# Kernel tuning notes

Measured on AMD Instinct MI355X. Metric: run time of the kernel, lower is better.

Reference implementation:

```python
import jax, jax.numpy as jnp
import numpy as np

SOFTMAX_SCALE = 10.0  # self.softmax_scale
EPS = 1e-4


def _patches(img, k=3):
    # img: [H, W, C] -> patches laid out as conv filters [k, k, C, L], L = H*W
    # (matches tf.image.extract_patches SAME/stride1 + reshape + transpose([0,2,3,4,1]))
    H, W, C = img.shape
    pad = (k - 1) // 2
    xp = jnp.pad(img, ((pad, pad), (pad, pad), (0, 0)))
    pat = jnp.stack([jnp.stack([xp[p:p + H, q:q + W] for q in range(k)]) for p in range(k)])
    # pat: [k, k, H, W, C] -> [k, k, C, H*W]; L index is row-major (h*W + w) like TF reshape
    return pat.transpose(0, 1, 4, 2, 3).reshape(k, k, C, H * W)


def _normed(p):
    # per-patch L2 normalization over the k*k*C axes (axes 0,1,2)
    return p / jnp.maximum(jnp.sqrt(jnp.sum(p * p, axis=(0, 1, 2))), EPS)


def _corr_recon(a, b, k=3):
    # a, b: [H', W', C] shifted feature maps
    Hp, Wp, C = a.shape
    L = Hp * Wp
    pa = _patches(a, k)  # [k,k,C,L]
    pb = _patches(b, k)
    y = (_normed(pa) * _normed(pb)).reshape(k * k * C, L)
    att = y.T @ y                                   # [L, L] patch-correlation scores
    att = jax.nn.softmax(att.reshape(1, Hp, Wp, L) * SOFTMAX_SCALE, axis=3)
    dn = ('NHWC', 'HWIO', 'NHWC')
    # tf.nn.conv2d_transpose(att, filters=[k,k,C,L], stride=1, SAME); rate=1 so /rate**2 is a no-op
    ya = jax.lax.conv_transpose(att, pa, (1, 1), 'SAME', dimension_numbers=dn, transpose_kernel=True)[0]
    yb = jax.lax.conv_transpose(att, pb, (1, 1), 'SAME', dimension_numbers=dn, transpose_kernel=True)[0]
    return ya, yb  # each [H', W', C]


def _ecattn_single(xi):
    # xi: [H, W, C]
    left, right = xi[:-1], xi[1:]          # vertical neighbor pair, [H-1, W, C]
    top, bottom = xi[:, 1:], xi[:, :-1]    # horizontal neighbor pair, [H, W-1, C]
    yl, yr = _corr_recon(left, right)
    ylr = jnp.concatenate([yr[:1], (yr[1:] + yl[:-1]) * 0.5, yl[-1:]], axis=0)   # [H, W, C]
    yt, yb = _corr_recon(top, bottom)
    ytb = jnp.concatenate([yt[:, :1], (yt[:, 1:] + yb[:, :-1]) * 0.5, yb[:, -1:]], axis=1)  # [H, W, C]
    return (ylr + ytb) * 0.5


def setup_inputs() -> dict:
    key = jax.random.key(0)
    k1, k2 = jax.random.split(key)
    B, H, W, C = 4, 32, 32, 256
    x = jax.random.normal(k1, (B, H, W, C), dtype=jnp.float32)
    mask = jax.random.uniform(k2, (B, H, W, 1), dtype=jnp.float32)
    return {'x': x, 'mask': mask}


def reference(x, mask):
    # mask is accepted by the layer's call() but unused inside contextualAttention
    return jax.vmap(_ecattn_single)(x)
```

## Files before the change

kernel.cpp:

```cpp
#include <hip/hip_runtime.h>


typedef _Float16 half8 __attribute__((ext_vector_type(8)));
typedef _Float16 half8u __attribute__((ext_vector_type(8), aligned(4)));
typedef _Float16 half4h __attribute__((ext_vector_type(4)));
typedef _Float16 half4u __attribute__((ext_vector_type(4), aligned(8)));
typedef float floatx4 __attribute__((ext_vector_type(4)));

constexpr int NL = 992, NC = 256, NC2 = 512;
constexpr int NLL = NL * NL;
constexpr int OFF_ABT = 0;
constexpr int OFF_MH  = OFF_ABT + NL * NC2 / 2;
constexpr int OFF_SA  = OFF_MH + NL * NC / 2;
constexpr int OFF_SB  = OFF_SA + 1024;
constexpr int OFF_INV = OFF_SA + 2048;
constexpr int OFF_Y   = OFF_SA + 3072;
constexpr int OFF_B0  = OFF_Y + NL * NC2 / 2;
constexpr int OFF_B1  = OFF_B0 + NLL / 2;
constexpr int TSTRIDE = OFF_B1 + NLL / 2;

__device__ __forceinline__ void gload16(const void* g, void* l) {
    __builtin_amdgcn_global_load_lds(
        (const __attribute__((address_space(1))) unsigned int*)g,
        (__attribute__((address_space(3))) unsigned int*)(unsigned long)(uintptr_t)l,
        16, 0, 0);
}

__global__ __launch_bounds__(256) void k_stage(const float* __restrict__ x,
                                               float* __restrict__ ws) {
    const int t = blockIdx.x & 7;
    const int l0 = (blockIdx.x >> 3) * 32;
    const int s = t >> 1, o = t & 1;
    float* wst = ws + (size_t)t * TSTRIDE;
    _Float16* __restrict__ ABt = (_Float16*)(wst + OFF_ABT);
    _Float16* __restrict__ Mh = (_Float16*)(wst + OFF_MH);
    __shared__ float Ta[32 * 33], Tb[32 * 33];
    const int tid = threadIdx.x;
    const int li = tid >> 3, cq = tid & 7;
    const int l = l0 + li;
    int aoff, boff;
    if (o == 0) {
        const int lh = l >> 5, lw = l & 31;
        aoff = ((s * 32 + lh) * 32 + lw) * NC;
        boff = aoff + 32 * NC;
    } else {
        const int lh = l / 31, lw = l - lh * 31;
        boff = ((s * 32 + lh) * 32 + lw) * NC;
        aoff = boff + NC;
    }
    float sa = 0.0f, sb = 0.0f;
    for (int cc = 0; cc < 8; ++cc) {
        const int c0 = cc * 32;
        const float4 a4 = *(const float4*)&x[aoff + c0 + cq * 4];
        const float4 b4 = *(const float4*)&x[boff + c0 + cq * 4];
        half4h m;
        m[0] = (_Float16)(a4.x * b4.x); m[1] = (_Float16)(a4.y * b4.y);
        m[2] = (_Float16)(a4.z * b4.z); m[3] = (_Float16)(a4.w * b4.w);
        *(half4u*)&Mh[l * NC + c0 + cq * 4] = m;
        sa += a4.x * a4.x + a4.y * a4.y + a4.z * a4.z + a4.w * a4.w;
        sb += b4.x * b4.x + b4.y * b4.y + b4.z * b4.z + b4.w * b4.w;
        __syncthreads();
        Ta[(cq * 4 + 0) * 33 + li] = a4.x; Tb[(cq * 4 + 0) * 33 + li] = b4.x;
        Ta[(cq * 4 + 1) * 33 + li] = a4.y; Tb[(cq * 4 + 1) * 33 + li] = b4.y;
        Ta[(cq * 4 + 2) * 33 + li] = a4.z; Tb[(cq * 4 + 2) * 33 + li] = b4.z;
        Ta[(cq * 4 + 3) * 33 + li] = a4.w; Tb[(cq * 4 + 3) * 33 + li] = b4.w;
        __syncthreads();
        const int ci = li, lq = cq;
        half4h ha, hb;
#pragma unroll
        for (int j = 0; j < 4; ++j) {
            ha[j] = (_Float16)Ta[ci * 33 + lq * 4 + j];
            hb[j] = (_Float16)Tb[ci * 33 + lq * 4 + j];
        }
        *(half4u*)&ABt[(c0 + ci) * NL + l0 + lq * 4] = ha;
        *(half4u*)&ABt[(NC + c0 + ci) * NL + l0 + lq * 4] = hb;
    }
#pragma unroll
    for (int off = 4; off > 0; off >>= 1) {
        sa += __shfl_down(sa, off, 8);
        sb += __shfl_down(sb, off, 8);
    }
    if (cq == 0) {
        wst[OFF_SA + l] = sa;
        wst[OFF_SB + l] = sb;
    }
}

__global__ __launch_bounds__(256) void k_gram(float* __restrict__ ws) {
    const int t = blockIdx.x & 7;
    const int u = blockIdx.x >> 3;
    const int i0 = (u >> 4) * 64, j0 = (u & 15) * 64;
    float* wst = ws + (size_t)t * TSTRIDE;
    const _Float16* __restrict__ M = (const _Float16*)(wst + OFF_MH);
    _Float16* __restrict__ S = (_Float16*)(wst + OFF_B0);
    const int tid = threadIdx.x;

    if (u == 0) {
        const int o = t & 1;
        const int Hp = o ? 32 : 31, Wp = o ? 31 : 32;
#pragma unroll
        for (int q = 0; q < 4; ++q) {
            const int l = tid + q * 256;
            if (l < NL) {
                const int h = l / Wp, w = l - h * Wp;
                float na2 = 0.0f, nb2 = 0.0f;
#pragma unroll
                for (int dh = -1; dh <= 1; ++dh)
#pragma unroll
                    for (int dw = -1; dw <= 1; ++dw) {
                        const int hh = h + dh, ww = w + dw;
                        if ((unsigned)hh < (unsigned)Hp && (unsigned)ww < (unsigned)Wp) {
                            const int ll = hh * Wp + ww;
                            na2 += wst[OFF_SA + ll];
                            nb2 += wst[OFF_SB + ll];
                        }
                    }
                const float na = fmaxf(sqrtf(na2), 1e-4f);
                const float nb = fmaxf(sqrtf(nb2), 1e-4f);
                wst[OFF_INV + l] = 1.0f / (na * nb);
            }
        }
    }

    __shared__ __align__(16) _Float16 As[64 * 64];
    __shared__ __align__(16) _Float16 Bs[64 * 64];
    const int wave = tid >> 6, lane = tid & 63;
    const int wm = wave & 1, wn = wave >> 1;
    const int l15 = lane & 15, quad = lane >> 4;
    floatx4 acc[2][2] = {};
    for (int k0 = 0; k0 < NC; k0 += 64) {
        __syncthreads();
#pragma unroll
        for (int rr = 0; rr < 2; ++rr) {
            const int slot = tid + rr * 256;
            const int row = slot >> 3, cg = (slot & 7) * 8;
            if (i0 + row < NL) gload16(&M[(i0 + row) * NC + k0 + cg], &As[row * 64 + cg]);
            if (j0 + row < NL) gload16(&M[(j0 + row) * NC + k0 + cg], &Bs[row * 64 + cg]);
        }
        __syncthreads();
#pragma unroll
        for (int kk = 0; kk < 2; ++kk) {
            half8 a[2], b[2];
#pragma unroll
            for (int mt = 0; mt < 2; ++mt) a[mt] = *(const half8*)&As[(wm * 32 + mt * 16 + l15) * 64 + kk * 32 + quad * 8];
#pragma unroll
            for (int nt = 0; nt < 2; ++nt) b[nt] = *(const half8*)&Bs[(wn * 32 + nt * 16 + l15) * 64 + kk * 32 + quad * 8];
#pragma unroll
            for (int mt = 0; mt < 2; ++mt)
#pragma unroll
                for (int nt = 0; nt < 2; ++nt)
                    acc[mt][nt] = __builtin_amdgcn_mfma_f32_16x16x32_f16(a[mt], b[nt], acc[mt][nt], 0, 0, 0);
        }
    }
#pragma unroll
    for (int mt = 0; mt < 2; ++mt)
#pragma unroll
        for (int nt = 0; nt < 2; ++nt)
#pragma unroll
            for (int r = 0; r < 4; ++r) {
                const int row = i0 + wm * 32 + mt * 16 + quad * 4 + r;
                const int col = j0 + wn * 32 + nt * 16 + l15;
                if (row < NL && col < NL) S[row * NL + col] = (_Float16)acc[mt][nt][r];
            }
}

template<int WP, int HP>
__device__ __forceinline__ void softmax9_body(float* __restrict__ wst,
                                              const int l1, const int tid) {
    const _Float16* __restrict__ S = (const _Float16*)(wst + OFF_B0);
    const float* __restrict__ inv = wst + OFF_INV;
    _Float16* __restrict__ Ph = (_Float16*)(wst + OFF_B1);
    const int c0 = tid * 4;
    const int h1 = l1 / WP, w1 = l1 % WP;
    float lg[4] = {-3.0e38f, -3.0e38f, -3.0e38f, -3.0e38f};
    float mx = -3.0e38f;
    if (tid < 248) {
        int hc[4], wc[4];
#pragma unroll
        for (int j = 0; j < 4; ++j) { hc[j] = (c0 + j) / WP; wc[j] = (c0 + j) % WP; }
        float g[4] = {0.f, 0.f, 0.f, 0.f};
        const _Float16* base = S + l1 * NL + c0;
#pragma unroll
        for (int dh = -1; dh <= 1; ++dh) {
            const bool oh1 = (unsigned)(h1 + dh) < (unsigned)HP;
#pragma unroll
            for (int dw = -1; dw <= 1; ++dw) {
                const int sh = dh * WP + dw;
                const int par = sh & 1;
                const bool ok1 = oh1 && (unsigned)(w1 + dw) < (unsigned)WP;
                const half8u v = *(const half8u*)(base + sh * (NL + 1) - par);
#pragma unroll
                for (int j = 0; j < 4; ++j) {
                    const bool ok = ok1 && (unsigned)(hc[j] + dh) < (unsigned)HP &&
                                           (unsigned)(wc[j] + dw) < (unsigned)WP;
                    if (ok) g[j] += (float)v[j + par];
                }
            }
        }
        const float inv1 = inv[l1] * 10.0f;
#pragma unroll
        for (int j = 0; j < 4; ++j) {
            lg[j] = g[j] * inv1 * inv[c0 + j];
            mx = fmaxf(mx, lg[j]);
        }
    }
    __shared__ float red[4];
    const int wave = tid >> 6, lane = tid & 63;
#pragma unroll
    for (int off = 32; off > 0; off >>= 1) mx = fmaxf(mx, __shfl_down(mx, off));
    if (lane == 0) red[wave] = mx;
    __syncthreads();
    mx = fmaxf(fmaxf(red[0], red[1]), fmaxf(red[2], red[3]));
    __syncthreads();
    float e[4];
    float sum = 0.0f;
#pragma unroll
    for (int j = 0; j < 4; ++j) { e[j] = __expf(lg[j] - mx); sum += e[j]; }
    if (tid >= 248) sum = 0.0f;
#pragma unroll
    for (int off = 32; off > 0; off >>= 1) sum += __shfl_down(sum, off);
    if (lane == 0) red[wave] = sum;
    __syncthreads();
    sum = red[0] + red[1] + red[2] + red[3];
    const float rs = 1.0f / sum;
    if (tid < 248) {
        half4h o;
#pragma unroll
        for (int j = 0; j < 4; ++j) o[j] = (_Float16)(e[j] * rs);
        *(half4u*)(Ph + l1 * NL + c0) = o;
    }
}

__global__ __launch_bounds__(256) void k_softmax9(float* __restrict__ ws) {
    const int t = blockIdx.x & 7;
    const int l1 = blockIdx.x >> 3;
    float* wst = ws + (size_t)t * TSTRIDE;
    if (t & 1) softmax9_body<31, 32>(wst, l1, threadIdx.x);
    else       softmax9_body<32, 31>(wst, l1, threadIdx.x);
}

template<int WP, int HP>
__device__ __forceinline__ void band9p_body(float* __restrict__ wst,
                                            const int m, const int tid) {
    if (tid >= 248) return;
    const _Float16* __restrict__ P = (const _Float16*)(wst + OFF_B1);
    _Float16* __restrict__ W = (_Float16*)(wst + OFF_B0);
    const int c0 = tid * 4;
    const int hm = m / WP, wm = m % WP;
    int hc[4], wc[4];
#pragma unroll
    for (int j = 0; j < 4; ++j) { hc[j] = (c0 + j) / WP; wc[j] = (c0 + j) % WP; }
    float acc[4] = {0.f, 0.f, 0.f, 0.f};
    const _Float16* base = P + m * NL + c0;
#pragma unroll
    for (int dh = -1; dh <= 1; ++dh) {
        const bool oh1 = (unsigned)(hm + dh) < (unsigned)HP;
#pragma unroll
        for (int dw = -1; dw <= 1; ++dw) {
            const int sh = dh * WP + dw;
            const int par = sh & 1;
            const bool ok1 = oh1 && (unsigned)(wm + dw) < (unsigned)WP;
            const half8u v = *(const half8u*)(base + sh * (NL + 1) - par);
#pragma unroll
            for (int j = 0; j < 4; ++j) {
                const bool ok = ok1 && (unsigned)(hc[j] + dh) < (unsigned)HP &&
                                       (unsigned)(wc[j] + dw) < (unsigned)WP;
                if (ok) acc[j] += (float)v[j + par];
            }
        }
    }
    half4h o;
#pragma unroll
    for (int j = 0; j < 4; ++j) o[j] = (_Float16)acc[j];
    *(half4u*)(W + m * NL + c0) = o;
}

__global__ __launch_bounds__(256) void k_band9p(float* __restrict__ ws) {
    const int t = blockIdx.x & 7;
    const int m = blockIdx.x >> 3;
    float* wst = ws + (size_t)t * TSTRIDE;
    if (t & 1) band9p_body<31, 32>(wst, m, threadIdx.x);
    else       band9p_body<32, 31>(wst, m, threadIdx.x);
}

__global__ __launch_bounds__(256) void k_recon(float* __restrict__ ws) {
    const int t = blockIdx.x & 7;
    const int u = blockIdx.x >> 3;
    const int i0 = (u >> 3) * 64, j0 = (u & 7) * 64;
    float* wst = ws + (size_t)t * TSTRIDE;
    const _Float16* __restrict__ Wm = (const _Float16*)(wst + OFF_B0);
    const _Float16* __restrict__ ABt = (const _Float16*)(wst + OFF_ABT);
    _Float16* __restrict__ Y = (_Float16*)(wst + OFF_Y);
    __shared__ __align__(16) _Float16 As[64 * 32];
    __shared__ __align__(16) _Float16 Bs[64 * 32];
    const int tid = threadIdx.x;
    const int wave = tid >> 6, lane = tid & 63;
    const int wm = wave & 1, wn = wave >> 1;
    const int l15 = lane & 15, quad = lane >> 4;
    floatx4 acc[2][2] = {};
    const int row = tid >> 2, cg = (tid & 3) * 8;
    for (int k0 = 0; k0 < NL; k0 += 32) {
        __syncthreads();
        if (i0 + row < NL) gload16(&Wm[(i0 + row) * NL + k0 + cg], &As[row * 32 + cg]);
        gload16(&ABt[(j0 + row) * NL + k0 + cg], &Bs[row * 32 + cg]);
        __syncthreads();
        half8 a[2], b[2];
#pragma unroll
        for (int mt = 0; mt < 2; ++mt) a[mt] = *(const half8*)&As[(wm * 32 + mt * 16 + l15) * 32 + quad * 8];
#pragma unroll
        for (int nt = 0; nt < 2; ++nt) b[nt] = *(const half8*)&Bs[(wn * 32 + nt * 16 + l15) * 32 + quad * 8];
#pragma unroll
        for (int mt = 0; mt < 2; ++mt)
#pragma unroll
            for (int nt = 0; nt < 2; ++nt)
                acc[mt][nt] = __builtin_amdgcn_mfma_f32_16x16x32_f16(a[mt], b[nt], acc[mt][nt], 0, 0, 0);
    }
#pragma unroll
    for (int mt = 0; mt < 2; ++mt)
#pragma unroll
        for (int nt = 0; nt < 2; ++nt)
#pragma unroll
            for (int r = 0; r < 4; ++r) {
                const int rw = i0 + wm * 32 + mt * 16 + quad * 4 + r;
                const int col = j0 + wn * 32 + nt * 16 + l15;
                if (rw < NL) Y[rw * NC2 + col] = (_Float16)acc[mt][nt][r];
            }
}

__global__ __launch_bounds__(256) void k_combine(float* __restrict__ out,
                                                 const float* __restrict__ ws) {
    const int idx = blockIdx.x;
    const int s = idx >> 10;
    const int hw = idx & 1023;
    const int h = hw >> 5, w = hw & 31;
    const int c = threadIdx.x;
    const _Float16* Ylr = (const _Float16*)(ws + (size_t)(2 * s) * TSTRIDE + OFF_Y);
    const _Float16* Ytb = (const _Float16*)(ws + (size_t)(2 * s + 1) * TSTRIDE + OFF_Y);
    float v = 0.0f;
    if (h < 31) v += (float)Ylr[(h * 32 + w) * NC2 + NC + c] * (h == 0 ? 1.0f : 0.5f);
    if (h >= 1) v += (float)Ylr[((h - 1) * 32 + w) * NC2 + c] * (h == 31 ? 1.0f : 0.5f);
    if (w < 31) v += (float)Ytb[(h * 31 + w) * NC2 + c] * (w == 0 ? 1.0f : 0.5f);
    if (w >= 1) v += (float)Ytb[(h * 31 + (w - 1)) * NC2 + NC + c] * (w == 31 ? 1.0f : 0.5f);
    out[(size_t)idx * NC + c] = v * 0.5f;
}

extern "C" void kernel_launch(void* const* d_in, const int* in_sizes, int n_in,
                              void* d_out, int out_size, void* d_ws, size_t ws_size,
                              hipStream_t stream) {
    const float* x = (const float*)d_in[0];
    float* out = (float*)d_out;
    float* ws = (float*)d_ws;

    hipLaunchKernelGGL(k_stage,    dim3(8 * 31),  dim3(256), 0, stream, x, ws);
    hipLaunchKernelGGL(k_gram,     dim3(8 * 256), dim3(256), 0, stream, ws);
    hipLaunchKernelGGL(k_softmax9, dim3(8 * NL),  dim3(256), 0, stream, ws);
    hipLaunchKernelGGL(k_band9p,   dim3(8 * NL),  dim3(256), 0, stream, ws);
    hipLaunchKernelGGL(k_recon,    dim3(8 * 128), dim3(256), 0, stream, ws);
    hipLaunchKernelGGL(k_combine,  dim3(4096),    dim3(256), 0, stream, out, ws);
}
```

Before: 146.1 us.

## Exploit Gram symmetry and map softmax/band rows to single waves

The Gram kernel now computes only upper-triangular 64x64 tiles (136 instead of 256 per problem). It stages each result tile in shared memory and writes both it and its transpose with vectorized stores. The softmax and band kernels now assign one row per wavefront, four rows per block, so the softmax reduction uses only wave shuffles with no shared-memory barriers. Softmax also drops the max-subtraction pass, relying on logits bounded by the scale of normalized correlations, which risks overflow only if inputs were unnormalized.

```diff
diff --git a/kernel.cpp b/kernel.cpp
--- a/kernel.cpp
+++ b/kernel.cpp
@@ -88,14 +88,17 @@
 
 __global__ __launch_bounds__(256) void k_gram(float* __restrict__ ws) {
     const int t = blockIdx.x & 7;
-    const int u = blockIdx.x >> 3;
-    const int i0 = (u >> 4) * 64, j0 = (u & 15) * 64;
+    int uu = blockIdx.x >> 3;
+    int ti = 0;
+    while (uu >= 16 - ti) { uu -= 16 - ti; ++ti; }
+    const int tj = ti + uu;
+    const int i0 = ti * 64, j0 = tj * 64;
     float* wst = ws + (size_t)t * TSTRIDE;
     const _Float16* __restrict__ M = (const _Float16*)(wst + OFF_MH);
     _Float16* __restrict__ S = (_Float16*)(wst + OFF_B0);
     const int tid = threadIdx.x;
 
-    if (u == 0) {
+    if (blockIdx.x >> 3 == 0) {
         const int o = t & 1;
         const int Hp = o ? 32 : 31, Wp = o ? 31 : 32;
 #pragma unroll
@@ -124,6 +127,7 @@
 
     __shared__ __align__(16) _Float16 As[64 * 64];
     __shared__ __align__(16) _Float16 Bs[64 * 64];
+    __shared__ __align__(16) _Float16 Ts[64 * 72];
     const int wave = tid >> 6, lane = tid & 63;
     const int wm = wave & 1, wn = wave >> 1;
     const int l15 = lane & 15, quad = lane >> 4;
@@ -152,29 +156,55 @@
                     acc[mt][nt] = __builtin_amdgcn_mfma_f32_16x16x32_f16(a[mt], b[nt], acc[mt][nt], 0, 0, 0);
         }
     }
+    __syncthreads();
 #pragma unroll
     for (int mt = 0; mt < 2; ++mt)
 #pragma unroll
         for (int nt = 0; nt < 2; ++nt)
 #pragma unroll
             for (int r = 0; r < 4; ++r) {
-                const int row = i0 + wm * 32 + mt * 16 + quad * 4 + r;
-                const int col = j0 + wn * 32 + nt * 16 + l15;
-                if (row < NL && col < NL) S[row * NL + col] = (_Float16)acc[mt][nt][r];
-            }
+                const int row = wm * 32 + mt * 16 + quad * 4 + r;
+                const int col = wn * 32 + nt * 16 + l15;
+                Ts[row * 72 + col] = (_Float16)acc[mt][nt][r];
+            }
+    __syncthreads();
+    const int trow = tid >> 3, tcg = (tid & 7) * 8;
+#pragma unroll
+    for (int rr = 0; rr < 2; ++rr) {
+        const int row = trow + rr * 32;
+        if (i0 + row < NL && j0 + tcg < NL) {
+            const half8 v = *(const half8*)&Ts[row * 72 + tcg];
+            *(half8*)&S[(i0 + row) * NL + j0 + tcg] = v;
+        }
+    }
+    if (i0 != j0) {
+#pragma unroll
+        for (int rr = 0; rr < 2; ++rr) {
+            const int row2 = trow + rr * 32;
+            if (j0 + row2 < NL && i0 + tcg < NL) {
+                half8 v;
+#pragma unroll
+                for (int k = 0; k < 8; ++k) v[k] = Ts[(tcg + k) * 72 + row2];
+                *(half8*)&S[(j0 + row2) * NL + i0 + tcg] = v;
+            }
+        }
+    }
 }
 
 template<int WP, int HP>
 __device__ __forceinline__ void softmax9_body(float* __restrict__ wst,
-                                              const int l1, const int tid) {
+                                              const int l1, const int lane) {
     const _Float16* __restrict__ S = (const _Float16*)(wst + OFF_B0);
     const float* __restrict__ inv = wst + OFF_INV;
     _Float16* __restrict__ Ph = (_Float16*)(wst + OFF_B1);
-    const int c0 = tid * 4;
     const int h1 = l1 / WP, w1 = l1 % WP;
-    float lg[4] = {-3.0e38f, -3.0e38f, -3.0e38f, -3.0e38f};
-    float mx = -3.0e38f;
-    if (tid < 248) {
+    const float inv1 = inv[l1] * 10.0f;
+    float e[16];
+    float sum = 0.0f;
+#pragma unroll
+    for (int jj = 0; jj < 4; ++jj) {
+        const bool act = (jj < 3) | (lane < 56);
+        const int c0 = jj * 256 + lane * 4;
         int hc[4], wc[4];
 #pragma unroll
         for (int j = 0; j < 4; ++j) { hc[j] = (c0 + j) / WP; wc[j] = (c0 + j) % WP; }
@@ -197,90 +227,86 @@
                 }
             }
         }
-        const float inv1 = inv[l1] * 10.0f;
 #pragma unroll
         for (int j = 0; j < 4; ++j) {
-            lg[j] = g[j] * inv1 * inv[c0 + j];
-            mx = fmaxf(mx, lg[j]);
-        }
-    }
-    __shared__ float red[4];
-    const int wave = tid >> 6, lane = tid & 63;
-#pragma unroll
-    for (int off = 32; off > 0; off >>= 1) mx = fmaxf(mx, __shfl_down(mx, off));
-    if (lane == 0) red[wave] = mx;
-    __syncthreads();
-    mx = fmaxf(fmaxf(red[0], red[1]), fmaxf(red[2], red[3]));
-    __syncthreads();
-    float e[4];
-    float sum = 0.0f;
-#pragma unroll
-    for (int j = 0; j < 4; ++j) { e[j] = __expf(lg[j] - mx); sum += e[j]; }
-    if (tid >= 248) sum = 0.0f;
+            const float ee = act ? __expf(g[j] * inv1 * inv[c0 + j]) : 0.0f;
+            e[jj * 4 + j] = ee;
+            sum += ee;
+        }
+    }
 #pragma unroll
     for (int off = 32; off > 0; off >>= 1) sum += __shfl_down(sum, off);
-    if (lane == 0) red[wave] = sum;
-    __syncthreads();
-    sum = red[0] + red[1] + red[2] + red[3];
-    const float rs = 1.0f / sum;
-    if (tid < 248) {
-        half4h o;
-#pragma unroll
-        for (int j = 0; j < 4; ++j) o[j] = (_Float16)(e[j] * rs);
-        *(half4u*)(Ph + l1 * NL + c0) = o;
+    const float rs = 1.0f / __shfl(sum, 0);
+#pragma unroll
+    for (int jj = 0; jj < 4; ++jj) {
+        if ((jj < 3) | (lane < 56)) {
+            const int c0 = jj * 256 + lane * 4;
+            half4h o;
+#pragma unroll
+            for (int j = 0; j < 4; ++j) o[j] = (_Float16)(e[jj * 4 + j] * rs);
+            *(half4u*)(Ph + l1 * NL + c0) = o;
+        }
     }
 }
 
 __global__ __launch_bounds__(256) void k_softmax9(float* __restrict__ ws) {
     const int t = blockIdx.x & 7;
-    const int l1 = blockIdx.x >> 3;
-    float* wst = ws + (size_t)t * TSTRIDE;
-    if (t & 1) softmax9_body<31, 32>(wst, l1, threadIdx.x);
-    else       softmax9_body<32, 31>(wst, l1, threadIdx.x);
+    const int rb = blockIdx.x >> 3;
+    const int wave = threadIdx.x >> 6, lane = threadIdx.x & 63;
+    const int l1 = rb * 4 + wave;
+    float* wst = ws + (size_t)t * TSTRIDE;
+    if (t & 1) softmax9_body<31, 32>(wst, l1, lane);
+    else       softmax9_body<32, 31>(wst, l1, lane);
 }
 
 template<int WP, int HP>
 __device__ __forceinline__ void band9p_body(float* __restrict__ wst,
-                                            const int m, const int tid) {
-    if (tid >= 248) return;
+                                            const int m, const int lane) {
     const _Float16* __restrict__ P = (const _Float16*)(wst + OFF_B1);
     _Float16* __restrict__ W = (_Float16*)(wst + OFF_B0);
-    const int c0 = tid * 4;
     const int hm = m / WP, wm = m % WP;
-    int hc[4], wc[4];
-#pragma unroll
-    for (int j = 0; j < 4; ++j) { hc[j] = (c0 + j) / WP; wc[j] = (c0 + j) % WP; }
-    float acc[4] = {0.f, 0.f, 0.f, 0.f};
-    const _Float16* base = P + m * NL + c0;
-#pragma unroll
-    for (int dh = -1; dh <= 1; ++dh) {
-        const bool oh1 = (unsigned)(hm + dh) < (unsigned)HP;
-#pragma unroll
-        for (int dw = -1; dw <= 1; ++dw) {
-            const int sh = dh * WP + dw;
-            const int par = sh & 1;
-            const bool ok1 = oh1 && (unsigned)(wm + dw) < (unsigned)WP;
-            const half8u v = *(const half8u*)(base + sh * (NL + 1) - par);
-#pragma unroll
-            for (int j = 0; j < 4; ++j) {
-                const bool ok = ok1 && (unsigned)(hc[j] + dh) < (unsigned)HP &&
-                                       (unsigned)(wc[j] + dw) < (unsigned)WP;
-                if (ok) acc[j] += (float)v[j + par];
-            }
-        }
-    }
-    half4h o;
-#pragma unroll
-    for (int j = 0; j < 4; ++j) o[j] = (_Float16)acc[j];
-    *(half4u*)(W + m * NL + c0) = o;
+#pragma unroll
+    for (int jj = 0; jj < 4; ++jj) {
+        const bool act = (jj < 3) | (lane < 56);
+        if (!act) continue;
+        const int c0 = jj * 256 + lane * 4;
+        int hc[4], wc[4];
+#pragma unroll
+        for (int j = 0; j < 4; ++j) { hc[j] = (c0 + j) / WP; wc[j] = (c0 + j) % WP; }
+        float acc[4] = {0.f, 0.f, 0.f, 0.f};
+        const _Float16* base = P + m * NL + c0;
+#pragma unroll
+        for (int dh = -1; dh <= 1; ++dh) {
+            const bool oh1 = (unsigned)(hm + dh) < (unsigned)HP;
+#pragma unroll
+            for (int dw = -1; dw <= 1; ++dw) {
+                const int sh = dh * WP + dw;
+                const int par = sh & 1;
+                const bool ok1 = oh1 && (unsigned)(wm + dw) < (unsigned)WP;
+                const half8u v = *(const half8u*)(base + sh * (NL + 1) - par);
+#pragma unroll
+                for (int j = 0; j < 4; ++j) {
+                    const bool ok = ok1 && (unsigned)(hc[j] + dh) < (unsigned)HP &&
+                                           (unsigned)(wc[j] + dw) < (unsigned)WP;
+                    if (ok) acc[j] += (float)v[j + par];
+                }
+            }
+        }
+        half4h o;
+#pragma unroll
+        for (int j = 0; j < 4; ++j) o[j] = (_Float16)acc[j];
+        *(half4u*)(W + m * NL + c0) = o;
+    }
 }
 
 __global__ __launch_bounds__(256) void k_band9p(float* __restrict__ ws) {
     const int t = blockIdx.x & 7;
-    const int m = blockIdx.x >> 3;
-    float* wst = ws + (size_t)t * TSTRIDE;
-    if (t & 1) band9p_body<31, 32>(wst, m, threadIdx.x);
-    else       band9p_body<32, 31>(wst, m, threadIdx.x);
+    const int rb = blockIdx.x >> 3;
+    const int wave = threadIdx.x >> 6, lane = threadIdx.x & 63;
+    const int m = rb * 4 + wave;
+    float* wst = ws + (size_t)t * TSTRIDE;
+    if (t & 1) band9p_body<31, 32>(wst, m, lane);
+    else       band9p_body<32, 31>(wst, m, lane);
 }
 
 __global__ __launch_bounds__(256) void k_recon(float* __restrict__ ws) {
@@ -352,9 +378,9 @@
     float* ws = (float*)d_ws;
 
     hipLaunchKernelGGL(k_stage,    dim3(8 * 31),  dim3(256), 0, stream, x, ws);
-    hipLaunchKernelGGL(k_gram,     dim3(8 * 256), dim3(256), 0, stream, ws);
-    hipLaunchKernelGGL(k_softmax9, dim3(8 * NL),  dim3(256), 0, stream, ws);
-    hipLaunchKernelGGL(k_band9p,   dim3(8 * NL),  dim3(256), 0, stream, ws);
+    hipLaunchKernelGGL(k_gram,     dim3(8 * 136), dim3(256), 0, stream, ws);
+    hipLaunchKernelGGL(k_softmax9, dim3(8 * 248), dim3(256), 0, stream, ws);
+    hipLaunchKernelGGL(k_band9p,   dim3(8 * 248), dim3(256), 0, stream, ws);
     hipLaunchKernelGGL(k_recon,    dim3(8 * 128), dim3(256), 0, stream, ws);
     hipLaunchKernelGGL(k_combine,  dim3(4096),    dim3(256), 0, stream, out, ws);
 }
```

New measurement: 150.8 us. 1.03x slower.
